# Kernel tuning notes

Hardware: AMD Instinct MI355X
Metric: run time of the kernel (lower is better)

The kernel has to match this reference:

```python
import jax, jax.numpy as jnp
import numpy as np

GRID_SIZE = 64
SPLINE_ORDER = 3
NUM_BASIS = GRID_SIZE + SPLINE_ORDER - 1  # 66
GRID_MIN, GRID_MAX = -1.0, 1.0
EPS = 1e-7
B, IN_F, OUT_F = 4096, 256, 256


def setup_inputs() -> dict:
    key = jax.random.key(0)
    k1, k2, k3, k4 = jax.random.split(key, 4)
    x = jax.random.normal(k1, (B, IN_F), dtype=jnp.float32)
    base_weight = jax.random.normal(k2, (IN_F, OUT_F), dtype=jnp.float32) * (1.0 / np.sqrt(IN_F))
    scale = 1.0 / np.sqrt(NUM_BASIS)
    spline_weight = jax.random.uniform(k3, (IN_F, OUT_F, NUM_BASIS), dtype=jnp.float32, minval=-scale, maxval=scale)
    spline_scaler = jax.random.uniform(k4, (IN_F, OUT_F), dtype=jnp.float32)
    return {"x": x, "base_weight": base_weight, "spline_weight": spline_weight, "spline_scaler": spline_scaler}


def _spline_basis(x):
    # normalize to [0,1], map onto grid coordinate
    x_c = jnp.clip(x, GRID_MIN, GRID_MAX)
    x_norm = (x_c - GRID_MIN) / (GRID_MAX - GRID_MIN + EPS)
    x_scaled = x_norm * (GRID_SIZE - 1)
    grid_idx = jnp.clip(jnp.floor(x_scaled), 0.0, GRID_SIZE - SPLINE_ORDER)
    local_x = x_scaled - grid_idx                                  # [B, in]
    centers = jnp.linspace(0.0, 1.0, NUM_BASIS, dtype=jnp.float32)  # [nb]
    sigma = 1.0 / NUM_BASIS
    bv = jnp.exp(-jnp.square(local_x[..., None] - centers) / (2.0 * sigma * sigma))  # [B, in, nb]
    # (safe_mode clip is skipped at inference: training falsy)
    bv = bv / (jnp.sum(bv, axis=-1, keepdims=True) + EPS)
    return bv


def reference(x, base_weight, spline_weight, spline_scaler):
    base_out = x @ base_weight                                     # [B, out]
    basis = _spline_basis(x)                                       # [B, in, nb]
    # sum over basis then over in_features: same math as the expanded
    # elementwise-product/sum chain in the original call()
    spline_out = jnp.einsum('bik,iok->bo', basis, spline_weight)   # [B, out]
    scaling = jnp.mean(jnp.maximum(spline_scaler, EPS), axis=0)    # [out]
    return base_out + spline_out * scaling
```

## Files before the change

### kernel.cpp

```cpp
#include <hip/hip_runtime.h>
#include <stdint.h>


#define IN_F 256
#define OUT_F 256
#define NB 66
#define KP 80
#define APAD 88
#define KSPLIT 8
#define SLABS 32
#define BM 128
#define NTHREADS 512

typedef __attribute__((ext_vector_type(8))) short bf16x8;
typedef __attribute__((ext_vector_type(16))) float f32x16;

__device__ __forceinline__ unsigned int f2bf(float f) {
  unsigned int u = __float_as_uint(f);
  u += 0x7FFFu + ((u >> 16) & 1u);
  return u >> 16;
}

__global__ void kan_scale8(const float* __restrict__ sca, float* __restrict__ wsp) {
  const int o = threadIdx.x, b = blockIdx.x;
  float s = 0.0f;
  #pragma unroll
  for (int j = 0; j < 32; j++) {
    const int i = b * 32 + j;
    s += fmaxf(sca[(size_t)i * OUT_F + o], 1e-7f);
  }
  wsp[b * OUT_F + o] = s;
}

__global__ void kan_pack(const float* __restrict__ sw, const float* __restrict__ bw,
                         const float* __restrict__ wsp, unsigned short* __restrict__ wp2) {
  const int i = blockIdx.x, o = threadIdx.x;
  float sc = 0.0f;
  #pragma unroll
  for (int b = 0; b < 8; b++) sc += wsp[b * OUT_F + o];
  sc *= (1.0f / 256.0f);
  const float2* src = (const float2*)(sw + ((size_t)i * OUT_F + o) * NB);
  float v[80];
  #pragma unroll
  for (int j = 0; j < 33; j++) {
    float2 t2 = src[j];
    v[2 * j] = t2.x * sc;
    v[2 * j + 1] = t2.y * sc;
  }
  v[66] = bw[(size_t)i * OUT_F + o];
  #pragma unroll
  for (int k = 67; k < 80; k++) v[k] = 0.0f;
  uint4* dst = (uint4*)wp2;
  #pragma unroll
  for (int g = 0; g < 10; g++) {
    uint4 u;
    unsigned int* up = (unsigned int*)&u;
    #pragma unroll
    for (int h = 0; h < 4; h++)
      up[h] = f2bf(v[g * 8 + 2 * h]) | (f2bf(v[g * 8 + 2 * h + 1]) << 16);
    dst[((size_t)i * 10 + g) * OUT_F + o] = u;
  }
}

__global__ __launch_bounds__(NTHREADS, 2) void kan_main(
    const float* __restrict__ x, const unsigned short* __restrict__ wp2,
    float* __restrict__ dst, int atomic_mode) {
  __shared__ unsigned short A[2][BM * APAD];

  const int t = threadIdx.x;
  const int lane = t & 63;
  const int w = t >> 6;
  const int ml = lane & 31;
  const int half = lane >> 5;
  const int mr = w >> 2;
  const int nc = w & 3;
  const int mblk = (int)blockIdx.x >> 3;
  const int kidx = (int)blockIdx.x & 7;
  const int b0 = mblk * BM;
  const int ibase = kidx * SLABS;

  const int rb = t >> 2;
  const int q = t & 3;
  const int ks = (q == 0) ? 0 : (q == 1) ? 24 : (q == 2) ? 40 : 64;
  const int len = (q & 1) ? 16 : 24;
  const int nchunk = len >> 3;

  const float* xrow = x + (size_t)(b0 + rb) * IN_F;
  const int boff = (nc * 64 + ml) * 8;

  bf16x8 breg[2][10];
  f32x16 acc[4] = {f32x16{}, f32x16{}, f32x16{}, f32x16{}};

#define LOADB(P, ISLAB)                                                        \
  {                                                                            \
    const unsigned short* bp =                                                 \
        wp2 + (size_t)(ISLAB) * (OUT_F * KP) + half * 2048 + boff;             \
    _Pragma("unroll") for (int kk = 0; kk < 5; kk++) {                         \
      breg[P][kk] = *(const bf16x8*)(bp + kk * 4096);                          \
      breg[P][5 + kk] = *(const bf16x8*)(bp + kk * 4096 + 256);                \
    }                                                                          \
  }

#define BASIS(BUFSEL, XVAL)                                                    \
  {                                                                            \
    const float xr_ = (XVAL);                                                  \
    const float xc_ = fminf(fmaxf(xr_, -1.0f), 1.0f);                          \
    const float xs_ = (xc_ + 1.0f) * (63.0f / (2.0f + 1e-7f));                 \
    const float tl_ = xs_ - fminf(floorf(xs_), 61.0f);                         \
    float e_[24];                                                              \
    float s_ = 0.0f;                                                           \
    _Pragma("unroll") for (int j = 0; j < 24; j++) {                           \
      const int k = ks + j;                                                    \
      const float d_ = tl_ - (float)k * (1.0f / 65.0f);                        \
      float ee = __expf(-2178.0f * d_ * d_);                                   \
      ee = (j < len && k < 66) ? ee : 0.0f;                                    \
      e_[j] = ee;                                                              \
      s_ += ee;                                                                \
    }                                                                          \
    s_ += __shfl_xor(s_, 1);                                                   \
    s_ += __shfl_xor(s_, 2);                                                   \
    const float r_ = __fdividef(1.0f, s_ + 1e-7f);                             \
    unsigned short* Ar = &A[BUFSEL][rb * APAD + ks];                           \
    _Pragma("unroll") for (int c = 0; c < 3; c++) {                            \
      if (c < nchunk) {                                                        \
        uint4 u;                                                               \
        unsigned int* up = (unsigned int*)&u;                                  \
        _Pragma("unroll") for (int h = 0; h < 4; h++) {                        \
          const int k0 = ks + c * 8 + h * 2;                                   \
          float f0 = e_[c * 8 + h * 2] * r_;                                   \
          float f1 = e_[c * 8 + h * 2 + 1] * r_;                               \
          f0 = (k0 == 66) ? xr_ : f0;                                          \
          f1 = (k0 + 1 == 66) ? xr_ : f1;                                      \
          up[h] = f2bf(f0) | (f2bf(f1) << 16);                                 \
        }                                                                      \
        *(uint4*)(Ar + c * 8) = u;                                             \
      }                                                                        \
    }                                                                          \
  }

#define MFMA_SLAB(CUR, P)                                                      \
  {                                                                            \
    const unsigned short* Ac = &A[CUR][0];                                     \
    _Pragma("unroll") for (int kk = 0; kk < 5; kk++) {                         \
      const int ko = kk * 16 + half * 8;                                       \
      bf16x8 a0 = *(const bf16x8*)(Ac + (mr * 64 + ml) * APAD + ko);           \
      bf16x8 a1 = *(const bf16x8*)(Ac + (mr * 64 + 32 + ml) * APAD + ko);      \
      acc[0] = __builtin_amdgcn_mfma_f32_32x32x16_bf16(a0, breg[P][kk], acc[0], 0, 0, 0);       \
      acc[1] = __builtin_amdgcn_mfma_f32_32x32x16_bf16(a0, breg[P][5 + kk], acc[1], 0, 0, 0);   \
      acc[2] = __builtin_amdgcn_mfma_f32_32x32x16_bf16(a1, breg[P][kk], acc[2], 0, 0, 0);       \
      acc[3] = __builtin_amdgcn_mfma_f32_32x32x16_bf16(a1, breg[P][5 + kk], acc[3], 0, 0, 0);   \
    }                                                                          \
  }

  BASIS(0, xrow[ibase]);
  LOADB(0, ibase);
  float xn = xrow[ibase + 1];
  __syncthreads();

#define STEP(II, P)                                                            \
  {                                                                            \
    if ((II) + 1 < SLABS) LOADB(1 - (P), ibase + (II) + 1);                    \
    MFMA_SLAB((II) & 1, P);                                                    \
    const float xc2 = xn;                                                      \
    if ((II) + 2 < SLABS) xn = xrow[ibase + (II) + 2];                         \
    if ((II) + 1 < SLABS) BASIS(((II) + 1) & 1, xc2);                          \
    __syncthreads();                                                           \
  }

  for (int ii = 0; ii < SLABS; ii += 2) {
    STEP(ii, 0);
    STEP(ii + 1, 1);
  }

  const int colb = nc * 64 + ml;
  if (atomic_mode) {
    #pragma unroll
    for (int mb = 0; mb < 2; mb++) {
      #pragma unroll
      for (int r = 0; r < 16; r++) {
        const int row = b0 + mr * 64 + mb * 32 + (r & 3) + 8 * (r >> 2) + 4 * half;
        atomicAdd(&dst[(size_t)row * OUT_F + colb], acc[mb * 2][r]);
        atomicAdd(&dst[(size_t)row * OUT_F + colb + 32], acc[mb * 2 + 1][r]);
      }
    }
  } else {
    float* pd = dst + (size_t)kidx * ((size_t)4096 * OUT_F);
    #pragma unroll
    for (int mb = 0; mb < 2; mb++) {
      #pragma unroll
      for (int r = 0; r < 16; r++) {
        const int row = b0 + mr * 64 + mb * 32 + (r & 3) + 8 * (r >> 2) + 4 * half;
        pd[(size_t)row * OUT_F + colb] = acc[mb * 2][r];
        pd[(size_t)row * OUT_F + colb + 32] = acc[mb * 2 + 1][r];
      }
    }
  }
}

__global__ void kan_reduce(const float* __restrict__ part, float* __restrict__ out) {
  const size_t j = ((size_t)blockIdx.x * 256 + threadIdx.x) * 4;
  float4 a = *(const float4*)(part + j);
  #pragma unroll
  for (int s = 1; s < 8; s++) {
    float4 b = *(const float4*)(part + (size_t)s * 1048576 + j);
    a.x += b.x; a.y += b.y; a.z += b.z; a.w += b.w;
  }
  *(float4*)(out + j) = a;
}

__global__ void kan_naive(const float* __restrict__ x, const float* __restrict__ bw,
                          const float* __restrict__ sw, const float* __restrict__ sca,
                          float* __restrict__ out) {
  const int o = threadIdx.x;
  const int b = blockIdx.x;
  float accb = 0.0f, accs = 0.0f, scl = 0.0f;
  for (int i = 0; i < IN_F; i++) {
    const float xraw = x[(size_t)b * IN_F + i];
    accb += xraw * bw[(size_t)i * OUT_F + o];
    scl += fmaxf(sca[(size_t)i * OUT_F + o], 1e-7f);
    const float xc = fminf(fmaxf(xraw, -1.0f), 1.0f);
    const float xs = (xc + 1.0f) * (63.0f / (2.0f + 1e-7f));
    const float tl = xs - fminf(floorf(xs), 61.0f);
    const int kc = (int)(tl * 65.0f + 0.5f);
    const int k0 = max(0, min(kc - 8, 50));
    float e[16]; float s = 0.0f;
    #pragma unroll
    for (int j = 0; j < 16; j++) {
      float d = tl - (float)(k0 + j) * (1.0f / 65.0f);
      e[j] = __expf(-2178.0f * d * d);
      s += e[j];
    }
    const float r = __fdividef(1.0f, s + 1e-7f);
    const float* wrow = sw + ((size_t)i * OUT_F + o) * NB + k0;
    float dot = 0.0f;
    #pragma unroll
    for (int j = 0; j < 16; j++) dot += e[j] * wrow[j];
    accs += dot * r;
  }
  out[(size_t)b * OUT_F + o] = accb + accs * (scl * (1.0f / 256.0f));
}

extern "C" void kernel_launch(void* const* d_in, const int* in_sizes, int n_in,
                              void* d_out, int out_size, void* d_ws, size_t ws_size,
                              hipStream_t stream) {
  const float* x   = (const float*)d_in[0];
  const float* bw  = (const float*)d_in[1];
  const float* sw  = (const float*)d_in[2];
  const float* sca = (const float*)d_in[3];
  float* out = (float*)d_out;

  const size_t WP2_BYTES  = (size_t)IN_F * OUT_F * KP * 2;
  const size_t WP_OFF     = 8192;
  const size_t PART_OFF   = WP_OFF + WP2_BYTES;
  const size_t PART_BYTES = (size_t)KSPLIT * 4096 * OUT_F * 4;

  if (ws_size >= PART_OFF + PART_BYTES) {
    float* wsp = (float*)d_ws;
    unsigned short* wp2 = (unsigned short*)((char*)d_ws + WP_OFF);
    float* part = (float*)((char*)d_ws + PART_OFF);
    kan_scale8<<<8, 256, 0, stream>>>(sca, wsp);
    kan_pack<<<256, 256, 0, stream>>>(sw, bw, wsp, wp2);
    kan_main<<<256, NTHREADS, 0, stream>>>(x, wp2, part, 0);
    kan_reduce<<<1024, 256, 0, stream>>>(part, out);
  } else if (ws_size >= PART_OFF) {
    float* wsp = (float*)d_ws;
    unsigned short* wp2 = (unsigned short*)((char*)d_ws + WP_OFF);
    hipMemsetAsync(d_out, 0, (size_t)out_size * sizeof(float), stream);
    kan_scale8<<<8, 256, 0, stream>>>(sca, wsp);
    kan_pack<<<256, 256, 0, stream>>>(sw, bw, wsp, wp2);
    kan_main<<<256, NTHREADS, 0, stream>>>(x, wp2, out, 1);
  } else {
    kan_naive<<<4096, 256, 0, stream>>>(x, bw, sw, sca, out);
  }
}
```

Before: 154.9 us.

## Compute only the 32 significant basis entries per row and re-tile warps

The basis stage now evaluates exponentials only for two 16-wide chunks around the Gaussian center. Half the threads compute them, and the other half zero-fill the remaining chunks and write the base-weight x term. This cuts per-slab transcendental work roughly from 66 to 32 exps per row. The MFMA warp tiling changes so each wave owns 32 columns and all 128 rows, halving B-register loads per wave. The pack kernel now stages spline weights through LDS for coalesced reads. Truncating the basis to 32 entries drops tiny tail values, which slightly changes numerics.

Result: slower. 214.3 us (+38.3%).

```diff
diff --git a/kernel.cpp b/kernel.cpp
--- a/kernel.cpp
+++ b/kernel.cpp
@@ -34,31 +34,48 @@
 
 __global__ void kan_pack(const float* __restrict__ sw, const float* __restrict__ bw,
                          const float* __restrict__ wsp, unsigned short* __restrict__ wp2) {
-  const int i = blockIdx.x, o = threadIdx.x;
-  float sc = 0.0f;
-  #pragma unroll
-  for (int b = 0; b < 8; b++) sc += wsp[b * OUT_F + o];
-  sc *= (1.0f / 256.0f);
-  const float2* src = (const float2*)(sw + ((size_t)i * OUT_F + o) * NB);
-  float v[80];
-  #pragma unroll
-  for (int j = 0; j < 33; j++) {
-    float2 t2 = src[j];
-    v[2 * j] = t2.x * sc;
-    v[2 * j + 1] = t2.y * sc;
-  }
-  v[66] = bw[(size_t)i * OUT_F + o];
-  #pragma unroll
-  for (int k = 67; k < 80; k++) v[k] = 0.0f;
-  uint4* dst = (uint4*)wp2;
-  #pragma unroll
-  for (int g = 0; g < 10; g++) {
-    uint4 u;
-    unsigned int* up = (unsigned int*)&u;
-    #pragma unroll
-    for (int h = 0; h < 4; h++)
-      up[h] = f2bf(v[g * 8 + 2 * h]) | (f2bf(v[g * 8 + 2 * h + 1]) << 16);
-    dst[((size_t)i * 10 + g) * OUT_F + o] = u;
+  __shared__ float S[128 * 68 + 64];
+  __shared__ float sc[256];
+  const int t = threadIdx.x, i = blockIdx.x;
+  {
+    float s = 0.0f;
+    #pragma unroll
+    for (int b = 0; b < 8; b++) s += wsp[b * OUT_F + t];
+    sc[t] = s * (1.0f / 256.0f);
+  }
+  uint4* wp2u4 = (uint4*)wp2;
+  for (int hf = 0; hf < 2; hf++) {
+    __syncthreads();
+    const float* src = sw + ((size_t)i * 256 + hf * 128) * NB;
+    #pragma unroll
+    for (int r2 = 0; r2 < 33; r2++) {
+      const int idx = r2 * 256 + t;
+      const int o = idx / 66;
+      const int k = idx - o * 66;
+      S[o * 68 + k] = src[idx];
+    }
+    __syncthreads();
+    const int ol = t >> 1, hh = t & 1;
+    const int og = hf * 128 + ol;
+    const float scv = sc[og];
+    const float bwv = bw[(size_t)i * 256 + og];
+    #pragma unroll
+    for (int gg = 0; gg < 5; gg++) {
+      const int g = hh * 5 + gg;
+      const int kb = g * 8;
+      unsigned int u[4];
+      #pragma unroll
+      for (int j = 0; j < 4; j++) {
+        const int k0 = kb + 2 * j, k1 = k0 + 1;
+        float f0 = S[ol * 68 + k0] * scv;
+        float f1 = S[ol * 68 + k1] * scv;
+        f0 = (k0 < 66) ? f0 : ((k0 == 66) ? bwv : 0.0f);
+        f1 = (k1 < 66) ? f1 : ((k1 == 66) ? bwv : 0.0f);
+        u[j] = f2bf(f0) | (f2bf(f1) << 16);
+      }
+      uint4 v; v.x = u[0]; v.y = u[1]; v.z = u[2]; v.w = u[3];
+      wp2u4[((size_t)i * 10 + g) * 256 + og] = v;
+    }
   }
 }
 
@@ -72,126 +89,127 @@
   const int w = t >> 6;
   const int ml = lane & 31;
   const int half = lane >> 5;
-  const int mr = w >> 2;
-  const int nc = w & 3;
   const int mblk = (int)blockIdx.x >> 3;
   const int kidx = (int)blockIdx.x & 7;
   const int b0 = mblk * BM;
   const int ibase = kidx * SLABS;
 
-  const int rb = t >> 2;
-  const int q = t & 3;
-  const int ks = (q == 0) ? 0 : (q == 1) ? 24 : (q == 2) ? 40 : 64;
-  const int len = (q & 1) ? 16 : 24;
-  const int nchunk = len >> 3;
+  const int rb = (t & 255) >> 1;
+  const int hh = t & 1;
+  const bool heavy = (t < 256);
 
   const float* xrow = x + (size_t)(b0 + rb) * IN_F;
-  const int boff = (nc * 64 + ml) * 8;
-
-  bf16x8 breg[2][10];
+  const unsigned short* bbase = wp2 + (size_t)half * 2048 + (w * 32 + ml) * 8;
+
+  bf16x8 breg[2][5];
   f32x16 acc[4] = {f32x16{}, f32x16{}, f32x16{}, f32x16{}};
 
 #define LOADB(P, ISLAB)                                                        \
   {                                                                            \
-    const unsigned short* bp =                                                 \
-        wp2 + (size_t)(ISLAB) * (OUT_F * KP) + half * 2048 + boff;             \
-    _Pragma("unroll") for (int kk = 0; kk < 5; kk++) {                         \
-      breg[P][kk] = *(const bf16x8*)(bp + kk * 4096);                          \
-      breg[P][5 + kk] = *(const bf16x8*)(bp + kk * 4096 + 256);                \
-    }                                                                          \
-  }
-
-#define BASIS(BUFSEL, XVAL)                                                    \
+    const unsigned short* bp = bbase + (size_t)(ISLAB) * (OUT_F * KP);         \
+    _Pragma("unroll") for (int kk = 0; kk < 5; kk++)                           \
+        breg[P][kk] = *(const bf16x8*)(bp + kk * 4096);                        \
+  }
+
+#define STAGE(BUF, XV)                                                         \
   {                                                                            \
-    const float xr_ = (XVAL);                                                  \
+    const float xr_ = (XV);                                                    \
     const float xc_ = fminf(fmaxf(xr_, -1.0f), 1.0f);                          \
     const float xs_ = (xc_ + 1.0f) * (63.0f / (2.0f + 1e-7f));                 \
     const float tl_ = xs_ - fminf(floorf(xs_), 61.0f);                         \
-    float e_[24];                                                              \
-    float s_ = 0.0f;                                                           \
-    _Pragma("unroll") for (int j = 0; j < 24; j++) {                           \
-      const int k = ks + j;                                                    \
-      const float d_ = tl_ - (float)k * (1.0f / 65.0f);                        \
-      float ee = __expf(-2178.0f * d_ * d_);                                   \
-      ee = (j < len && k < 66) ? ee : 0.0f;                                    \
-      e_[j] = ee;                                                              \
-      s_ += ee;                                                                \
-    }                                                                          \
-    s_ += __shfl_xor(s_, 1);                                                   \
-    s_ += __shfl_xor(s_, 2);                                                   \
-    const float r_ = __fdividef(1.0f, s_ + 1e-7f);                             \
-    unsigned short* Ar = &A[BUFSEL][rb * APAD + ks];                           \
-    _Pragma("unroll") for (int c = 0; c < 3; c++) {                            \
-      if (c < nchunk) {                                                        \
-        uint4 u;                                                               \
-        unsigned int* up = (unsigned int*)&u;                                  \
-        _Pragma("unroll") for (int h = 0; h < 4; h++) {                        \
-          const int k0 = ks + c * 8 + h * 2;                                   \
-          float f0 = e_[c * 8 + h * 2] * r_;                                   \
-          float f1 = e_[c * 8 + h * 2 + 1] * r_;                               \
-          f0 = (k0 == 66) ? xr_ : f0;                                          \
-          f1 = (k0 + 1 == 66) ? xr_ : f1;                                      \
-          up[h] = f2bf(f0) | (f2bf(f1) << 16);                                 \
-        }                                                                      \
-        *(uint4*)(Ar + c * 8) = u;                                             \
+    const int kc_ = (int)(tl_ * 65.0f + 0.5f);                                 \
+    const int c0_ = (min(max(kc_ - 8, 0), 50)) >> 4;                           \
+    unsigned short* Ar = &A[BUF][rb * APAD];                                   \
+    if (heavy) {                                                               \
+      const int kb = (c0_ + hh) * 16;                                          \
+      float vv[16];                                                            \
+      float s_ = 0.0f;                                                         \
+      _Pragma("unroll") for (int j = 0; j < 16; j++) {                         \
+        const float d_ = tl_ - (float)(kb + j) * (1.0f / 65.0f);               \
+        float ee = __expf(-2178.0f * d_ * d_);                                 \
+        ee = (kb + j < 66) ? ee : 0.0f;                                        \
+        vv[j] = ee;                                                            \
+        s_ += ee;                                                              \
+      }                                                                        \
+      s_ += __shfl_xor(s_, 1);                                                 \
+      const float r_ = __fdividef(1.0f, s_ + 1e-7f);                           \
+      unsigned int u[8];                                                       \
+      _Pragma("unroll") for (int j = 0; j < 8; j++) {                          \
+        float f0 = vv[2 * j] * r_;                                             \
+        float f1 = vv[2 * j + 1] * r_;                                         \
+        f0 = (kb + 2 * j == 66) ? xr_ : f0;                                    \
+        f1 = (kb + 2 * j + 1 == 66) ? xr_ : f1;                                \
+        u[j] = f2bf(f0) | (f2bf(f1) << 16);                                    \
+      }                                                                        \
+      uint4 v0, v1;                                                            \
+      v0.x = u[0]; v0.y = u[1]; v0.z = u[2]; v0.w = u[3];                      \
+      v1.x = u[4]; v1.y = u[5]; v1.z = u[6]; v1.w = u[7];                      \
+      *(uint4*)(Ar + kb) = v0;                                                 \
+      *(uint4*)(Ar + kb + 8) = v1;                                             \
+    } else {                                                                   \
+      const int f0_ = (c0_ == 0) ? 2 : 0;                                      \
+      const int f1_ = (c0_ <= 1) ? 3 : 1;                                      \
+      const int f2_ = (c0_ == 3) ? 2 : 4;                                      \
+      uint4 z; z.x = 0; z.y = 0; z.z = 0; z.w = 0;                             \
+      if (hh == 0) {                                                           \
+        *(uint4*)(Ar + f0_ * 16) = z;                                          \
+        *(uint4*)(Ar + f0_ * 16 + 8) = z;                                      \
+        *(uint4*)(Ar + f1_ * 16) = z;                                          \
+        *(uint4*)(Ar + f1_ * 16 + 8) = z;                                      \
+      } else {                                                                 \
+        uint4 a = z;                                                           \
+        a.y = (f2_ == 4) ? f2bf(xr_) : 0u;   \
+        *(uint4*)(Ar + f2_ * 16) = a;                                          \
+        *(uint4*)(Ar + f2_ * 16 + 8) = z;                                      \
       }                                                                        \
     }                                                                          \
   }
 
 #define MFMA_SLAB(CUR, P)                                                      \
   {                                                                            \
-    const unsigned short* Ac = &A[CUR][0];                                     \
+    const unsigned short* Ac = &A[CUR][ml * APAD + half * 8];                  \
     _Pragma("unroll") for (int kk = 0; kk < 5; kk++) {                         \
-      const int ko = kk * 16 + half * 8;                                       \
-      bf16x8 a0 = *(const bf16x8*)(Ac + (mr * 64 + ml) * APAD + ko);           \
-      bf16x8 a1 = *(const bf16x8*)(Ac + (mr * 64 + 32 + ml) * APAD + ko);      \
-      acc[0] = __builtin_amdgcn_mfma_f32_32x32x16_bf16(a0, breg[P][kk], acc[0], 0, 0, 0);       \
-      acc[1] = __builtin_amdgcn_mfma_f32_32x32x16_bf16(a0, breg[P][5 + kk], acc[1], 0, 0, 0);   \
-      acc[2] = __builtin_amdgcn_mfma_f32_32x32x16_bf16(a1, breg[P][kk], acc[2], 0, 0, 0);       \
-      acc[3] = __builtin_amdgcn_mfma_f32_32x32x16_bf16(a1, breg[P][5 + kk], acc[3], 0, 0, 0);   \
+      _Pragma("unroll") for (int mb = 0; mb < 4; mb++) {                       \
+        bf16x8 af = *(const bf16x8*)(Ac + mb * 32 * APAD + kk * 16);           \
+        acc[mb] = __builtin_amdgcn_mfma_f32_32x32x16_bf16(af, breg[P][kk],     \
+                                                          acc[mb], 0, 0, 0);  \
+      }                                                                        \
     }                                                                          \
   }
 
-  BASIS(0, xrow[ibase]);
+  STAGE(0, xrow[ibase]);
   LOADB(0, ibase);
   float xn = xrow[ibase + 1];
   __syncthreads();
 
-#define STEP(II, P)                                                            \
-  {                                                                            \
-    if ((II) + 1 < SLABS) LOADB(1 - (P), ibase + (II) + 1);                    \
-    MFMA_SLAB((II) & 1, P);                                                    \
-    const float xc2 = xn;                                                      \
-    if ((II) + 2 < SLABS) xn = xrow[ibase + (II) + 2];                         \
-    if ((II) + 1 < SLABS) BASIS(((II) + 1) & 1, xc2);                          \
-    __syncthreads();                                                           \
-  }
-
-  for (int ii = 0; ii < SLABS; ii += 2) {
-    STEP(ii, 0);
-    STEP(ii + 1, 1);
-  }
-
-  const int colb = nc * 64 + ml;
+  for (int ii = 0; ii < SLABS; ii++) {
+    const int cur = ii & 1;
+    if (ii + 1 < SLABS) LOADB(1 - cur, ibase + ii + 1);
+    MFMA_SLAB(cur, cur);
+    const float xc2 = xn;
+    if (ii + 2 < SLABS) xn = xrow[ibase + ii + 2];
+    if (ii + 1 < SLABS) STAGE(1 - cur, xc2);
+    __syncthreads();
+  }
+
+  const int colb = w * 32 + ml;
   if (atomic_mode) {
     #pragma unroll
-    for (int mb = 0; mb < 2; mb++) {
+    for (int mb = 0; mb < 4; mb++) {
       #pragma unroll
       for (int r = 0; r < 16; r++) {
-        const int row = b0 + mr * 64 + mb * 32 + (r & 3) + 8 * (r >> 2) + 4 * half;
-        atomicAdd(&dst[(size_t)row * OUT_F + colb], acc[mb * 2][r]);
-        atomicAdd(&dst[(size_t)row * OUT_F + colb + 32], acc[mb * 2 + 1][r]);
+        const int row = b0 + mb * 32 + (r & 3) + 8 * (r >> 2) + 4 * half;
+        atomicAdd(&dst[(size_t)row * OUT_F + colb], acc[mb][r]);
       }
     }
   } else {
     float* pd = dst + (size_t)kidx * ((size_t)4096 * OUT_F);
     #pragma unroll
-    for (int mb = 0; mb < 2; mb++) {
+    for (int mb = 0; mb < 4; mb++) {
       #pragma unroll
       for (int r = 0; r < 16; r++) {
-        const int row = b0 + mr * 64 + mb * 32 + (r & 3) + 8 * (r >> 2) + 4 * half;
-        pd[(size_t)row * OUT_F + colb] = acc[mb * 2][r];
-        pd[(size_t)row * OUT_F + colb + 32] = acc[mb * 2 + 1][r];
+        const int row = b0 + mb * 32 + (r & 3) + 8 * (r >> 2) + 4 * half;
+        pd[(size_t)row * OUT_F + colb] = acc[mb][r];
       }
     }
   }
```
